# Kernel tuning notes

Hardware: AMD Instinct MI355X
Metric: run time of the kernel (lower is better)

## Reference

```python
import jax, jax.numpy as jnp
import numpy as np

# ---- constants from the source module ----
NB = [[0,1,2,3],[0,1,4],[0,2,5],[0,3,6],[1,4,7],[2,5,8],[3,6,9],[4,7,10],[5,8,11],[6,9],[7,10],[8,11],[12,13,14,15],[12,13,16],[12,14,17],[12,15],[13,16,18],[14,17,19],[16,18,20],[17,19,21],[18,20,22],[19,21,23],[20,22],[21,23]]
PARENT = np.array([0,0,0,0,1,2,3,4,5,6,7,8,9,9,9,12,13,14,16,17,18,19,20,21])  # root parent sentinel handled separately
KJ, NV, PREG = 24, 6890, 200
LEN = np.array([len(n) for n in NB])
NBR_IDX = np.zeros((KJ,4), np.int32)
NBR_VALID = np.zeros((KJ,4), np.float32)
for k, n in enumerate(NB):
    NBR_IDX[k,:len(n)] = n; NBR_VALID[k,:len(n)] = 1.0
BETA_POS = np.zeros((KJ,17), np.float32); BETA_POS[np.arange(KJ), 4*LEN] = 1.0
SLICE_MASK = np.zeros((23,17), np.float32)
for j in range(23):
    SLICE_MASK[j,:4*LEN[j]+1] = 1.0  # self.K[j] has 4*len(NB[j])+1 rows
NBR_IDX = jnp.asarray(NBR_IDX); NBR_VALID = jnp.asarray(NBR_VALID)
BETA_POS = jnp.asarray(BETA_POS); SLICE_MASK = jnpp = jnp.asarray(SLICE_MASK)


def setup_inputs() -> dict:
    key = jax.random.key(0)
    ks = jax.random.split(key, 9)
    V = jax.random.normal(ks[0], (PREG, NV, 3), jnp.float32)
    T = jax.random.normal(ks[1], (PREG, NV, 3), jnp.float32)
    J = jax.random.normal(ks[2], (PREG, KJ, 3), jnp.float32)
    theta = 0.3 * jax.random.normal(ks[3], (PREG, 72), jnp.float32)
    W_prime = jax.random.uniform(ks[4], (NV, KJ), jnp.float32)
    W_i = jax.random.uniform(ks[5], (NV, KJ), jnp.float32)
    W_i = W_i / W_i.sum(axis=1, keepdims=True)
    A = jax.random.uniform(ks[6], (23, NV), jnp.float32)
    K_mats = 0.01 * jax.random.normal(ks[7], (23, 17, 3 * NV), jnp.float32)
    K_mats = K_mats * SLICE_MASK[:, :, None]  # zero rows beyond the ragged per-joint size
    beta_2 = jnp.ones((1,), jnp.float32)
    return {"V": V, "T": T, "J": J, "theta": theta, "W_prime": W_prime, "W_i": W_i, "A": A, "K_mats": K_mats, "beta_2": beta_2, "epoch": 1}


def _rodrigues(pose):  # pose: (K,3)
    angle = jnp.maximum(jnp.linalg.norm(pose, axis=1, keepdims=True), 1e-8)
    axis = pose / angle
    x, y, z = axis[:, 0], axis[:, 1], axis[:, 2]
    zero = jnp.zeros_like(x)
    skew = jnp.stack([zero, -z, y, z, zero, -x, -y, x, zero], axis=1).reshape(-1, 3, 3)
    outer = axis[:, :, None] * axis[:, None, :]
    c = jnp.cos(angle)[:, :, None]
    s = jnp.sin(angle)[:, :, None]
    eye = jnp.eye(3, dtype=pose.dtype)[None]
    return c * eye + (1.0 - c) * outer + s * skew


def _compute_G(pose72, Jp):  # pose72: (72,), Jp: (K,3) -> (K,4,4)
    R = _rodrigues(pose72.reshape(KJ, 3))
    t = Jp - jnp.concatenate([jnp.zeros((1, 3), Jp.dtype), Jp[PARENT[1:]]], axis=0)
    G_local = jnp.zeros((KJ, 4, 4), Jp.dtype)
    G_local = G_local.at[:, :3, :3].set(R).at[:, :3, 3].set(t).at[:, 3, 3].set(1.0)
    Gs = [G_local[0]]
    for i in range(1, KJ):  # fixed 24-joint kinematic tree
        Gs.append(Gs[PARENT[i]] @ G_local[i])
    G = jnp.stack(Gs, axis=0)
    off = jnp.einsum('kij,kj->ki', G[:, :3, :3], Jp)  # homogeneous w=0 -> rotation only
    return G.at[:, :3, 3].add(-off)


def _axis2quat(p):  # (M,3) -> (M,4)
    angle = jnp.sqrt(jnp.maximum(jnp.sum(p ** 2, axis=1), 1e-16))
    n = p / angle[:, None]
    s = jnp.sin(angle / 2)
    return jnp.stack([n[:, 0] * s, n[:, 1] * s, n[:, 2] * s, jnp.cos(angle / 2) - 1.0], axis=1)


def reference(V, T, J, theta, W_prime, W_i, A, K_mats, beta_2, epoch):
    P = V.shape[0]
    b2 = beta_2[0]
    # normalized skinning weights
    W_relu = jax.nn.relu(W_prime)
    W_change = W_relu / (W_relu.sum(axis=1, keepdims=True) + 1e-8)
    # per-pose global joint transforms
    G_prime = jax.vmap(_compute_G)(theta, J)  # (P,K,4,4)
    # quaternion features and blend-shape correction
    q = _axis2quat(theta.reshape(P * KJ, 3)).reshape(P, KJ, 4)
    qg = q[:, NBR_IDX, :] * NBR_VALID[None, :, :, None]       # (P,K,4,4) neighbor gather
    q17 = jnp.concatenate([qg.reshape(P, KJ, 16), jnp.zeros((P, KJ, 1), q.dtype)], axis=-1)
    q17 = q17 + BETA_POS[None] * b2                            # beta_2 at column 4*len
    qm = q17[:, 1:, :] * SLICE_MASK[None]                      # ragged slice q_ne[:, j+1, :lenK]
    contrib = jnp.einsum('pjl,jlm->pjm', qm, K_mats).reshape(P, 23, NV, 3)
    T_p = jnp.einsum('pjnc,jn->pnc', contrib, jax.nn.relu(A)) + T
    # linear blend skinning
    T_h = jnp.concatenate([T_p, jnp.ones((P, NV, 1), T_p.dtype)], axis=-1)
    transformed = jnp.einsum('pkij,pnj->pnki', G_prime[:, :, :3, :], T_h)  # (P,N,K,3)
    verts = jnp.einsum('nk,pnkc->pnc', W_change, transformed)
    # energies
    e = float(epoch)
    g_wi = 0.1 * np.exp(-0.1 * e)
    g_w = 0.002 * np.exp(-0.008 * e)
    g_a = 0.001 * np.exp(-0.008 * e)
    g_k = 0.1 * np.exp(-0.008 * e)
    E_D = jnp.sum((V - verts) ** 2)
    E_Wi = jnp.sum((W_change - W_i) ** 2)
    E_W = jnp.sum(jnp.abs(W_change))
    E_A = jnp.sum(jnp.abs(A))
    E_K = jnp.sum(jnp.sqrt(jnp.sum(K_mats ** 2, axis=(1, 2))))
    E = E_D + g_wi * E_Wi + g_w * E_W + g_a * E_A + g_k * E_K
    return (E, verts)
```

## Files before the change

kernel.cpp:

```cpp
#include <hip/hip_runtime.h>
#include <math.h>

#define KJ 24
#define NV 6890
#define PREG 200
#define M_TOT (NV*3)
#define KDIM 391
#define KPAD 416
#define TP_STRIDE 20672
#define NMT64 323
#define NSTAGE (NMT64*13)

#define EDP_OFF 0
#define EKP_OFF 5400
#define WIP_OFF 101984
#define EWP_OFF 102016
#define EAP_OFF 102048
#define RED_OFF 102080
#define G_OFF   102112
#define TP_OFF  159712
#define QBH_OFF_U 10903488
#define QBL_OFF_U 11009984
#define BTH_OFF_U 11116480
#define BTL_OFF_U 19716032
#define TP2_OFF 14157792

typedef __attribute__((ext_vector_type(8))) short short8;
typedef __attribute__((ext_vector_type(4))) float f32x4;
typedef __attribute__((ext_vector_type(4))) unsigned int u32x4;

__constant__ int c_PARENT[24] = {0,0,0,0,1,2,3,4,5,6,7,8,9,9,9,12,13,14,16,17,18,19,20,21};
__constant__ int c_DEPTH[24]  = {0,1,1,1,2,2,2,3,3,3,4,4,4,4,4,5,5,5,6,6,7,7,8,8};
__constant__ int c_LEN[24]    = {4,3,3,3,3,3,3,3,3,2,2,2,4,3,3,2,3,3,3,3,3,3,2,2};
__constant__ int c_NBR[24][4] = {
  {0,1,2,3},{0,1,4,0},{0,2,5,0},{0,3,6,0},{1,4,7,0},{2,5,8,0},{3,6,9,0},{4,7,10,0},
  {5,8,11,0},{6,9,0,0},{7,10,0,0},{8,11,0,0},{12,13,14,15},{12,13,16,0},{12,14,17,0},
  {12,15,0,0},{13,16,18,0},{14,17,19,0},{16,18,20,0},{17,19,21,0},{18,20,22,0},
  {19,21,23,0},{20,22,0,0},{21,23,0,0}};

__device__ __forceinline__ float waveReduce(float v) {
  #pragma unroll
  for (int off = 32; off > 0; off >>= 1) v += __shfl_down(v, off, 64);
  return v;
}
__device__ __forceinline__ unsigned short f2bf(float x) {
  union { float f; unsigned u; } v; v.f = x;
  unsigned r = v.u + 0x7FFFu + ((v.u >> 16) & 1u);
  return (unsigned short)(r >> 16);
}
__device__ __forceinline__ float bf2f(unsigned short h) {
  union { unsigned u; float f; } v; v.u = ((unsigned)h) << 16; return v.f;
}

__global__ __launch_bounds__(256) void kPre(const float* __restrict__ J,
                                            const float* __restrict__ theta,
                                            const float* __restrict__ beta2,
                                            const float* __restrict__ Wp,
                                            const float* __restrict__ Wi,
                                            const float* __restrict__ A,
                                            const float* __restrict__ K,
                                            float* __restrict__ ws) {
  unsigned short* qbh = (unsigned short*)ws + QBH_OFF_U;
  unsigned short* qbl = (unsigned short*)ws + QBL_OFF_U;
  int b = blockIdx.x;
  if (b < 50) {
    __shared__ float Gl[4][24][12];
    __shared__ float Gg[4][24][12];
    __shared__ float q[4][24][4];
    int w = threadIdx.x >> 6, t = threadIdx.x & 63;
    int p = b*4 + w;
    if (t < 24) {
      float x = theta[p*72 + 3*t + 0];
      float y = theta[p*72 + 3*t + 1];
      float z = theta[p*72 + 3*t + 2];
      float n2 = x*x + y*y + z*z;
      float ang = fmaxf(sqrtf(n2), 1e-8f);
      float ia = 1.f/ang;
      float ax = x*ia, ay = y*ia, az = z*ia;
      float c = cosf(ang), s = sinf(ang), C = 1.f - c;
      float jx = J[p*72+3*t], jy = J[p*72+3*t+1], jz = J[p*72+3*t+2];
      float tx = jx, ty = jy, tz = jz;
      if (t > 0) {
        int par = c_PARENT[t];
        tx -= J[p*72+3*par]; ty -= J[p*72+3*par+1]; tz -= J[p*72+3*par+2];
      }
      Gl[w][t][0]=c+C*ax*ax;   Gl[w][t][1]=C*ax*ay-s*az; Gl[w][t][2]=C*ax*az+s*ay; Gl[w][t][3]=tx;
      Gl[w][t][4]=C*ax*ay+s*az;Gl[w][t][5]=c+C*ay*ay;    Gl[w][t][6]=C*ay*az-s*ax; Gl[w][t][7]=ty;
      Gl[w][t][8]=C*ax*az-s*ay;Gl[w][t][9]=C*ay*az+s*ax; Gl[w][t][10]=c+C*az*az;   Gl[w][t][11]=tz;
      float ang2 = sqrtf(fmaxf(n2, 1e-16f));
      float inv2 = 1.f/ang2;
      float s2 = sinf(0.5f*ang2);
      q[w][t][0] = x*inv2*s2; q[w][t][1] = y*inv2*s2; q[w][t][2] = z*inv2*s2;
      q[w][t][3] = cosf(0.5f*ang2) - 1.f;
    }
    __syncthreads();
    for (int lev = 0; lev <= 8; lev++) {
      if (t < 24 && c_DEPTH[t] == lev) {
        if (lev == 0) {
          for (int i2 = 0; i2 < 12; i2++) Gg[w][0][i2] = Gl[w][0][i2];
        } else {
          int par = c_PARENT[t];
          for (int r = 0; r < 3; r++) {
            float g0 = Gg[w][par][r*4+0], g1 = Gg[w][par][r*4+1];
            float g2 = Gg[w][par][r*4+2], g3 = Gg[w][par][r*4+3];
            for (int c2 = 0; c2 < 4; c2++) {
              float v = g0*Gl[w][t][0+c2] + g1*Gl[w][t][4+c2] + g2*Gl[w][t][8+c2];
              if (c2 == 3) v += g3;
              Gg[w][t][r*4+c2] = v;
            }
          }
        }
      }
      __syncthreads();
    }
    if (t < 24) {
      float jx = J[p*72+3*t], jy = J[p*72+3*t+1], jz = J[p*72+3*t+2];
      float* gp = ws + G_OFF + p*288 + t*12;
      #pragma unroll
      for (int r = 0; r < 3; r++) {
        float off = Gg[w][t][r*4+0]*jx + Gg[w][t][r*4+1]*jy + Gg[w][t][r*4+2]*jz;
        Gg[w][t][r*4+3] -= off;
      }
      #pragma unroll
      for (int i2 = 0; i2 < 12; i2++) gp[i2] = Gg[w][t][i2];
    }
    __syncthreads();
    float b2 = beta2[0];
    for (int e = t; e < KDIM; e += 64) {
      int j = e / 17, l = e - 17*j;
      int k = j + 1;
      float val = 0.f;
      if (l < 4*c_LEN[j] + 1) {
        if (l < 16) {
          int sidx = l >> 2, cc = l & 3;
          if (sidx < c_LEN[k]) val = q[w][c_NBR[k][sidx]][cc];
        }
        if (l == 4*c_LEN[k]) val += b2;
      }
      unsigned short hi = f2bf(val);
      unsigned short lo = f2bf(val - bf2f(hi));
      qbh[p*KPAD + e] = hi;
      qbl[p*KPAD + e] = lo;
    }
    for (int e = KDIM + t; e < KPAD; e += 64) {
      qbh[p*KPAD + e] = 0; qbl[p*KPAD + e] = 0;
    }
  } else if (b < 77) {
    int d = b - 50;
    int t = threadIdx.x;
    int n = d*256 + t;
    float ewi = 0.f, ew = 0.f, ea = 0.f;
    if (n < NV) {
      float wv[24]; float sum = 0.f;
      const float4* wp4 = (const float4*)(Wp + n*24);
      #pragma unroll
      for (int i = 0; i < 6; i++) {
        float4 v4 = wp4[i];
        wv[4*i+0] = fmaxf(v4.x, 0.f); wv[4*i+1] = fmaxf(v4.y, 0.f);
        wv[4*i+2] = fmaxf(v4.z, 0.f); wv[4*i+3] = fmaxf(v4.w, 0.f);
        sum += wv[4*i+0]+wv[4*i+1]+wv[4*i+2]+wv[4*i+3];
      }
      float inv = 1.f/(sum + 1e-8f);
      #pragma unroll
      for (int k = 0; k < 24; k++) {
        float wc = wv[k]*inv;
        ew += fabsf(wc);
        float dd = wc - Wi[n*24+k];
        ewi += dd*dd;
      }
    }
    for (int i = d*256 + t; i < 23*NV; i += 27*256) ea += fabsf(A[i]);
    for (int i = d*256 + t; i < 56*KPAD; i += 27*256) {
      qbh[200*KPAD + i] = 0; qbl[200*KPAD + i] = 0;
    }
    __shared__ float red[3][4];
    int lane = t & 63, wv2 = t >> 6;
    ewi = waveReduce(ewi); ew = waveReduce(ew); ea = waveReduce(ea);
    if (lane == 0) { red[0][wv2] = ewi; red[1][wv2] = ew; red[2][wv2] = ea; }
    __syncthreads();
    if (t == 0) {
      ws[WIP_OFF + d] = red[0][0]+red[0][1]+red[0][2]+red[0][3];
      ws[EWP_OFF + d] = red[1][0]+red[1][1]+red[1][2]+red[1][3];
      ws[EAP_OFF + d] = red[2][0]+red[2][1]+red[2][2]+red[2][3];
    }
  } else {
    int flat = b - 77;
    int bx = flat % NMT64, by = flat / NMT64;
    int m0 = bx*64, kg0 = by*32;
    __shared__ unsigned short Sh[32*66];
    __shared__ unsigned short Sl[32*66];
    __shared__ float ek[23];
    int t = threadIdx.x;
    if (t < 23) ek[t] = 0.f;
    __syncthreads();
    int krow = t >> 3, mseg = (t & 7) * 8;
    int kg = kg0 + krow;
    int mm = m0 + mseg;
    float kv[8], wv[8]; float sq = 0.f;
    #pragma unroll
    for (int i = 0; i < 8; i++) { kv[i] = 0.f; wv[i] = 0.f; }
    if (kg < KDIM) {
      const float* kr = K + (size_t)kg*M_TOT + mm;
      if (mm + 7 < M_TOT) {
        float4 a4 = *(const float4*)kr; float4 b4 = *(const float4*)(kr+4);
        kv[0]=a4.x; kv[1]=a4.y; kv[2]=a4.z; kv[3]=a4.w;
        kv[4]=b4.x; kv[5]=b4.y; kv[6]=b4.z; kv[7]=b4.w;
      } else {
        #pragma unroll
        for (int i = 0; i < 8; i++) if (mm+i < M_TOT) kv[i] = kr[i];
      }
      int j = kg / 17;
      int nb = mm / 3;
      float av[4];
      #pragma unroll
      for (int i = 0; i < 4; i++)
        av[i] = (nb + i < NV) ? fmaxf(A[j*NV + nb + i], 0.f) : 0.f;
      #pragma unroll
      for (int i = 0; i < 8; i++) {
        float a = (mm+i < M_TOT) ? av[(mm+i)/3 - nb] : 0.f;
        wv[i] = kv[i]*a;
        sq = fmaf(kv[i], kv[i], sq);
      }
    }
    #pragma unroll
    for (int c = 0; c < 4; c++) {
      unsigned short h0 = f2bf(wv[2*c]),  h1 = f2bf(wv[2*c+1]);
      unsigned short l0 = f2bf(wv[2*c]   - bf2f(h0));
      unsigned short l1 = f2bf(wv[2*c+1] - bf2f(h1));
      *(unsigned*)&Sh[krow*66 + mseg + 2*c] = (unsigned)h0 | ((unsigned)h1 << 16);
      *(unsigned*)&Sl[krow*66 + mseg + 2*c] = (unsigned)l0 | ((unsigned)l1 << 16);
    }
    sq += __shfl_xor(sq, 1, 64);
    sq += __shfl_xor(sq, 2, 64);
    sq += __shfl_xor(sq, 4, 64);
    if ((t & 7) == 0 && kg < KDIM) atomicAdd(&ek[kg/17], sq);
    __syncthreads();
    int mrow = t >> 2, kq = t & 3;
    unsigned dh[4], dl[4];
    #pragma unroll
    for (int c2 = 0; c2 < 4; c2++) {
      unsigned short s0 = Sh[(kq*8 + 2*c2    )*66 + mrow];
      unsigned short s1 = Sh[(kq*8 + 2*c2 + 1)*66 + mrow];
      dh[c2] = (unsigned)s0 | ((unsigned)s1 << 16);
      unsigned short u0 = Sl[(kq*8 + 2*c2    )*66 + mrow];
      unsigned short u1 = Sl[(kq*8 + 2*c2 + 1)*66 + mrow];
      dl[c2] = (unsigned)u0 | ((unsigned)u1 << 16);
    }
    unsigned short* BtH = (unsigned short*)ws + BTH_OFF_U;
    unsigned short* BtL = (unsigned short*)ws + BTL_OFF_U;
    size_t o = (size_t)(m0 + mrow)*KPAD + kg0 + kq*8;
    *(u32x4*)(BtH + o) = (u32x4){dh[0], dh[1], dh[2], dh[3]};
    *(u32x4*)(BtL + o) = (u32x4){dl[0], dl[1], dl[2], dl[3]};
    if (t < 23) ws[EKP_OFF + t*NSTAGE + flat] = ek[t];
  }
}

template<int KS0, int NKS>
__device__ __forceinline__ void kb_body(const unsigned short* __restrict__ qbh,
                                        const unsigned short* __restrict__ qbl,
                                        const unsigned short* __restrict__ BtH,
                                        const unsigned short* __restrict__ BtL,
                                        short (*__restrict__ SBh)[64*40],
                                        short (*__restrict__ SBl)[64*40],
                                        float* __restrict__ TPd, int m0) {
  const int tid = threadIdx.x;
  const int w = tid >> 6, lane = tid & 63;
  const int r = lane & 15, qd = lane >> 4;

  f32x4 acc[4][4];
  #pragma unroll
  for (int h = 0; h < 4; h++)
    #pragma unroll
    for (int f = 0; f < 4; f++) acc[h][f] = (f32x4){0.f,0.f,0.f,0.f};

  int aofs[4];
  #pragma unroll
  for (int h = 0; h < 4; h++) aofs[h] = (w*64 + h*16 + r)*KPAD + KS0*32 + qd*8;

  const int srow = tid >> 2, sseg = tid & 3;
  const size_t gB = (size_t)(m0 + srow)*KPAD + KS0*32 + sseg*8;
  const int swr = srow*40 + sseg*8;

  short8 ah[2][4], al[2][4];
  short8 bsh[2], bsl[2];

  bsh[0] = *(const short8*)(BtH + gB);
  bsl[0] = *(const short8*)(BtL + gB);
  #pragma unroll
  for (int h = 0; h < 4; h++) {
    ah[0][h] = *(const short8*)(qbh + aofs[h]);
    al[0][h] = *(const short8*)(qbl + aofs[h]);
  }
  *(short8*)&SBh[0][swr] = bsh[0];
  *(short8*)&SBl[0][swr] = bsl[0];
  bsh[1] = *(const short8*)(BtH + gB + 32);
  bsl[1] = *(const short8*)(BtL + gB + 32);
  #pragma unroll
  for (int h = 0; h < 4; h++) {
    ah[1][h] = *(const short8*)(qbh + aofs[h] + 32);
    al[1][h] = *(const short8*)(qbl + aofs[h] + 32);
  }
  __syncthreads();

  #pragma unroll
  for (int ks = 0; ks < NKS; ks++) {
    const int cur = ks & 1, nxt = cur ^ 1;
    short8 bfh[4], bfl[4];
    #pragma unroll
    for (int f = 0; f < 4; f++) {
      bfh[f] = *(const short8*)&SBh[cur][(f*16 + r)*40 + qd*8];
      bfl[f] = *(const short8*)&SBl[cur][(f*16 + r)*40 + qd*8];
    }
    #pragma unroll
    for (int f = 0; f < 4; f++)
      #pragma unroll
      for (int h = 0; h < 4; h++) {
        acc[h][f] = __builtin_amdgcn_mfma_f32_16x16x32_bf16(ah[cur][h], bfh[f], acc[h][f], 0, 0, 0);
        acc[h][f] = __builtin_amdgcn_mfma_f32_16x16x32_bf16(ah[cur][h], bfl[f], acc[h][f], 0, 0, 0);
        acc[h][f] = __builtin_amdgcn_mfma_f32_16x16x32_bf16(al[cur][h], bfh[f], acc[h][f], 0, 0, 0);
      }
    if (ks + 1 < NKS) {
      *(short8*)&SBh[nxt][swr] = bsh[nxt];
      *(short8*)&SBl[nxt][swr] = bsl[nxt];
    }
    if (ks + 2 < NKS) {
      const int o = (ks + 2) * 32;
      bsh[cur] = *(const short8*)(BtH + gB + o);
      bsl[cur] = *(const short8*)(BtL + gB + o);
      #pragma unroll
      for (int h = 0; h < 4; h++) {
        ah[cur][h] = *(const short8*)(qbh + aofs[h] + o);
        al[cur][h] = *(const short8*)(qbl + aofs[h] + o);
      }
    }
    __syncthreads();
  }
  #pragma unroll
  for (int h = 0; h < 4; h++)
    #pragma unroll
    for (int f = 0; f < 4; f++)
      #pragma unroll
      for (int g = 0; g < 4; g++) {
        int p = w*64 + h*16 + qd*4 + g;
        if (p < PREG)
          TPd[(size_t)p*TP_STRIDE + m0 + f*16 + r] = acc[h][f][g];
      }
}

__global__ __launch_bounds__(256) void kB(float* __restrict__ ws) {
  __shared__ short SBh[2][64*40];
  __shared__ short SBl[2][64*40];
  const unsigned short* qbh = (const unsigned short*)ws + QBH_OFF_U;
  const unsigned short* qbl = (const unsigned short*)ws + QBL_OFF_U;
  const unsigned short* BtH = (const unsigned short*)ws + BTH_OFF_U;
  const unsigned short* BtL = (const unsigned short*)ws + BTL_OFF_U;
  const int m0 = blockIdx.x * 64;
  if (blockIdx.y == 0)
    kb_body<0, 7>(qbh, qbl, BtH, BtL, SBh, SBl, ws + TP_OFF, m0);
  else
    kb_body<7, 6>(qbh, qbl, BtH, BtL, SBh, SBl, ws + TP2_OFF, m0);
}

__global__ __launch_bounds__(256) void kC(const float* __restrict__ V,
                                          const float* __restrict__ T,
                                          const float* __restrict__ Wp,
                                          const float* __restrict__ ws,
                                          float* __restrict__ out) {
  int p = blockIdx.y;
  int n = blockIdx.x*256 + threadIdx.x;
  const float* __restrict__ gp = ws + G_OFF + (size_t)p*288;
  __shared__ float tmp[4];
  float ed = 0.f;
  if (n < NV) {
    float wv[24]; float sum = 0.f;
    const float4* wp4 = (const float4*)(Wp + n*24);
    #pragma unroll
    for (int i = 0; i < 6; i++) {
      float4 v4 = wp4[i];
      wv[4*i+0] = fmaxf(v4.x, 0.f); wv[4*i+1] = fmaxf(v4.y, 0.f);
      wv[4*i+2] = fmaxf(v4.z, 0.f); wv[4*i+3] = fmaxf(v4.w, 0.f);
      sum += wv[4*i+0]+wv[4*i+1]+wv[4*i+2]+wv[4*i+3];
    }
    float inv = 1.f/(sum + 1e-8f);
    float M[12];
    #pragma unroll
    for (int i = 0; i < 12; i++) M[i] = 0.f;
    #pragma unroll
    for (int k = 0; k < 24; k++) {
      float wc = wv[k];
      #pragma unroll
      for (int i = 0; i < 12; i++)
        M[i] = fmaf(wc, gp[k*12 + i], M[i]);
    }
    #pragma unroll
    for (int i = 0; i < 12; i++) M[i] *= inv;
    size_t tb = (size_t)p*M_TOT + 3*n;
    size_t pb = (size_t)p*TP_STRIDE + 3*n;
    float t0 = ws[TP_OFF + pb + 0] + ws[TP2_OFF + pb + 0] + T[tb + 0];
    float t1 = ws[TP_OFF + pb + 1] + ws[TP2_OFF + pb + 1] + T[tb + 1];
    float t2 = ws[TP_OFF + pb + 2] + ws[TP2_OFF + pb + 2] + T[tb + 2];
    float v0 = M[0]*t0 + M[1]*t1 + M[2]*t2  + M[3];
    float v1 = M[4]*t0 + M[5]*t1 + M[6]*t2  + M[7];
    float v2 = M[8]*t0 + M[9]*t1 + M[10]*t2 + M[11];
    out[1+tb+0] = v0; out[1+tb+1] = v1; out[1+tb+2] = v2;
    float d0 = V[tb+0]-v0, d1 = V[tb+1]-v1, d2 = V[tb+2]-v2;
    ed = d0*d0 + d1*d1 + d2*d2;
  }
  ed = waveReduce(ed);
  int lane = threadIdx.x & 63, w = threadIdx.x >> 6;
  if (lane == 0) tmp[w] = ed;
  __syncthreads();
  if (threadIdx.x == 0)
    ((float*)ws)[EDP_OFF + blockIdx.y*27 + blockIdx.x] = tmp[0]+tmp[1]+tmp[2]+tmp[3];
}

__global__ __launch_bounds__(256) void kF1(float* __restrict__ ws) {
  __shared__ float sb[4];
  int b = blockIdx.x, t = threadIdx.x, lane = t & 63, w = t >> 6;
  if (b < 23) {
    float s = 0.f;
    for (int i = t; i < NSTAGE; i += 256) s += ws[EKP_OFF + b*NSTAGE + i];
    s = waveReduce(s);
    if (lane == 0) sb[w] = s;
    __syncthreads();
    if (t == 0) ws[RED_OFF + b] = sb[0]+sb[1]+sb[2]+sb[3];
  } else if (b == 23) {
    float s = 0.f;
    for (int i = t; i < 5400; i += 256) s += ws[EDP_OFF + i];
    s = waveReduce(s);
    if (lane == 0) sb[w] = s;
    __syncthreads();
    if (t == 0) ws[RED_OFF + 23] = sb[0]+sb[1]+sb[2]+sb[3];
  } else {
    if (w == 0) {
      float s = (lane < 27) ? ws[WIP_OFF + lane] : 0.f;
      s = waveReduce(s);
      if (lane == 0) ws[RED_OFF + 24] = s;
    } else if (w == 1) {
      float s = (lane < 27) ? ws[EWP_OFF + lane] : 0.f;
      s = waveReduce(s);
      if (lane == 0) ws[RED_OFF + 25] = s;
    } else if (w == 2) {
      float s = (lane < 27) ? ws[EAP_OFF + lane] : 0.f;
      s = waveReduce(s);
      if (lane == 0) ws[RED_OFF + 26] = s;
    }
  }
}

__global__ void kF2(const int* __restrict__ epoch, const float* __restrict__ ws,
                    float* __restrict__ out) {
  int t = threadIdx.x;
  float s = (t < 23) ? sqrtf(ws[RED_OFF + t]) : 0.f;
  s = waveReduce(s);
  if (t == 0) {
    float e    = (float)epoch[0];
    float g_wi = 0.1f   * expf(-0.1f  * e);
    float g_w  = 0.002f * expf(-0.008f* e);
    float g_a  = 0.001f * expf(-0.008f* e);
    float g_k  = 0.1f   * expf(-0.008f* e);
    out[0] = ws[RED_OFF+23] + g_wi*ws[RED_OFF+24] + g_w*ws[RED_OFF+25]
           + g_a*ws[RED_OFF+26] + g_k*s;
  }
}

extern "C" void kernel_launch(void* const* d_in, const int* in_sizes, int n_in,
                              void* d_out, int out_size, void* d_ws, size_t ws_size,
                              hipStream_t stream) {
  const float* V     = (const float*)d_in[0];
  const float* T     = (const float*)d_in[1];
  const float* J     = (const float*)d_in[2];
  const float* theta = (const float*)d_in[3];
  const float* Wp    = (const float*)d_in[4];
  const float* Wi    = (const float*)d_in[5];
  const float* A     = (const float*)d_in[6];
  const float* K     = (const float*)d_in[7];
  const float* b2    = (const float*)d_in[8];
  const int*   epoch = (const int*)d_in[9];
  float* out = (float*)d_out;
  float* ws  = (float*)d_ws;

  hipLaunchKernelGGL(kPre, dim3(77 + NSTAGE), dim3(256), 0, stream,
                     J, theta, b2, Wp, Wi, A, K, ws);
  hipLaunchKernelGGL(kB,   dim3(NMT64, 2),    dim3(256), 0, stream, ws);
  hipLaunchKernelGGL(kC,   dim3(27, PREG),    dim3(256), 0, stream, V, T, Wp, ws, out);
  hipLaunchKernelGGL(kF1,  dim3(25),          dim3(256), 0, stream, ws);
  hipLaunchKernelGGL(kF2,  dim3(1),           dim3(64),  0, stream, epoch, ws, out);
}
```

Baseline: 182.2 us.

## Widen GEMM tile to 128 columns, split K three ways, batch poses in skinning

The MFMA GEMM kernel now uses 512-thread blocks covering 128 output columns, with 8 waves each handling 32 pose rows. The K dimension is split into three partial sums instead of two, which adds a third partial buffer. The skinning kernel processes 8 poses per block and reuses the loaded blend weights across them, cutting the grid and the partial energy count. The goal is more B-tile reuse and fewer redundant weight loads. The cost is extra partial-buffer traffic, and the tile no longer divides M evenly, so loads and stores need clamping and guards.

```diff
diff --git a/kernel.cpp b/kernel.cpp
--- a/kernel.cpp
+++ b/kernel.cpp
@@ -10,6 +10,7 @@
 #define TP_STRIDE 20672
 #define NMT64 323
 #define NSTAGE (NMT64*13)
+#define NMT128 162
 
 #define EDP_OFF 0
 #define EKP_OFF 5400
@@ -24,6 +25,7 @@
 #define BTH_OFF_U 11116480
 #define BTL_OFF_U 19716032
 #define TP2_OFF 14157792
+#define TP3_OFF 19449824
 
 typedef __attribute__((ext_vector_type(8))) short short8;
 typedef __attribute__((ext_vector_type(4))) float f32x4;
@@ -260,34 +262,35 @@
                                         const unsigned short* __restrict__ qbl,
                                         const unsigned short* __restrict__ BtH,
                                         const unsigned short* __restrict__ BtL,
-                                        short (*__restrict__ SBh)[64*40],
-                                        short (*__restrict__ SBl)[64*40],
+                                        short (*__restrict__ SBh)[128*40],
+                                        short (*__restrict__ SBl)[128*40],
                                         float* __restrict__ TPd, int m0) {
   const int tid = threadIdx.x;
   const int w = tid >> 6, lane = tid & 63;
   const int r = lane & 15, qd = lane >> 4;
 
-  f32x4 acc[4][4];
-  #pragma unroll
-  for (int h = 0; h < 4; h++)
-    #pragma unroll
-    for (int f = 0; f < 4; f++) acc[h][f] = (f32x4){0.f,0.f,0.f,0.f};
-
-  int aofs[4];
-  #pragma unroll
-  for (int h = 0; h < 4; h++) aofs[h] = (w*64 + h*16 + r)*KPAD + KS0*32 + qd*8;
+  f32x4 acc[2][8];
+  #pragma unroll
+  for (int h = 0; h < 2; h++)
+    #pragma unroll
+    for (int f = 0; f < 8; f++) acc[h][f] = (f32x4){0.f,0.f,0.f,0.f};
+
+  int aofs[2];
+  #pragma unroll
+  for (int h = 0; h < 2; h++) aofs[h] = (w*32 + h*16 + r)*KPAD + KS0*32 + qd*8;
 
   const int srow = tid >> 2, sseg = tid & 3;
-  const size_t gB = (size_t)(m0 + srow)*KPAD + KS0*32 + sseg*8;
+  int grow = m0 + srow; if (grow > M_TOT + 1) grow = M_TOT + 1;
+  const size_t gB = (size_t)grow*KPAD + KS0*32 + sseg*8;
   const int swr = srow*40 + sseg*8;
 
-  short8 ah[2][4], al[2][4];
+  short8 ah[2][2], al[2][2];
   short8 bsh[2], bsl[2];
 
   bsh[0] = *(const short8*)(BtH + gB);
   bsl[0] = *(const short8*)(BtL + gB);
   #pragma unroll
-  for (int h = 0; h < 4; h++) {
+  for (int h = 0; h < 2; h++) {
     ah[0][h] = *(const short8*)(qbh + aofs[h]);
     al[0][h] = *(const short8*)(qbl + aofs[h]);
   }
@@ -296,7 +299,7 @@
   bsh[1] = *(const short8*)(BtH + gB + 32);
   bsl[1] = *(const short8*)(BtL + gB + 32);
   #pragma unroll
-  for (int h = 0; h < 4; h++) {
+  for (int h = 0; h < 2; h++) {
     ah[1][h] = *(const short8*)(qbh + aofs[h] + 32);
     al[1][h] = *(const short8*)(qbl + aofs[h] + 32);
   }
@@ -305,16 +308,16 @@
   #pragma unroll
   for (int ks = 0; ks < NKS; ks++) {
     const int cur = ks & 1, nxt = cur ^ 1;
-    short8 bfh[4], bfl[4];
-    #pragma unroll
-    for (int f = 0; f < 4; f++) {
+    short8 bfh[8], bfl[8];
+    #pragma unroll
+    for (int f = 0; f < 8; f++) {
       bfh[f] = *(const short8*)&SBh[cur][(f*16 + r)*40 + qd*8];
       bfl[f] = *(const short8*)&SBl[cur][(f*16 + r)*40 + qd*8];
     }
     #pragma unroll
-    for (int f = 0; f < 4; f++)
-      #pragma unroll
-      for (int h = 0; h < 4; h++) {
+    for (int f = 0; f < 8; f++)
+      #pragma unroll
+      for (int h = 0; h < 2; h++) {
         acc[h][f] = __builtin_amdgcn_mfma_f32_16x16x32_bf16(ah[cur][h], bfh[f], acc[h][f], 0, 0, 0);
         acc[h][f] = __builtin_amdgcn_mfma_f32_16x16x32_bf16(ah[cur][h], bfl[f], acc[h][f], 0, 0, 0);
         acc[h][f] = __builtin_amdgcn_mfma_f32_16x16x32_bf16(al[cur][h], bfh[f], acc[h][f], 0, 0, 0);
@@ -328,7 +331,7 @@
       bsh[cur] = *(const short8*)(BtH + gB + o);
       bsl[cur] = *(const short8*)(BtL + gB + o);
       #pragma unroll
-      for (int h = 0; h < 4; h++) {
+      for (int h = 0; h < 2; h++) {
         ah[cur][h] = *(const short8*)(qbh + aofs[h] + o);
         al[cur][h] = *(const short8*)(qbl + aofs[h] + o);
       }
@@ -336,29 +339,35 @@
     __syncthreads();
   }
   #pragma unroll
-  for (int h = 0; h < 4; h++)
-    #pragma unroll
-    for (int f = 0; f < 4; f++)
-      #pragma unroll
-      for (int g = 0; g < 4; g++) {
-        int p = w*64 + h*16 + qd*4 + g;
-        if (p < PREG)
-          TPd[(size_t)p*TP_STRIDE + m0 + f*16 + r] = acc[h][f][g];
-      }
-}
-
-__global__ __launch_bounds__(256) void kB(float* __restrict__ ws) {
-  __shared__ short SBh[2][64*40];
-  __shared__ short SBl[2][64*40];
+  for (int h = 0; h < 2; h++)
+    #pragma unroll
+    for (int f = 0; f < 8; f++) {
+      int mc = m0 + f*16 + r;
+      if (mc < TP_STRIDE) {
+        #pragma unroll
+        for (int g = 0; g < 4; g++) {
+          int p = w*32 + h*16 + qd*4 + g;
+          if (p < PREG)
+            TPd[(size_t)p*TP_STRIDE + mc] = acc[h][f][g];
+        }
+      }
+    }
+}
+
+__global__ __launch_bounds__(512) void kB(float* __restrict__ ws) {
+  __shared__ short SBh[2][128*40];
+  __shared__ short SBl[2][128*40];
   const unsigned short* qbh = (const unsigned short*)ws + QBH_OFF_U;
   const unsigned short* qbl = (const unsigned short*)ws + QBL_OFF_U;
   const unsigned short* BtH = (const unsigned short*)ws + BTH_OFF_U;
   const unsigned short* BtL = (const unsigned short*)ws + BTL_OFF_U;
-  const int m0 = blockIdx.x * 64;
+  const int m0 = blockIdx.x * 128;
   if (blockIdx.y == 0)
-    kb_body<0, 7>(qbh, qbl, BtH, BtL, SBh, SBl, ws + TP_OFF, m0);
+    kb_body<0, 5>(qbh, qbl, BtH, BtL, SBh, SBl, ws + TP_OFF, m0);
+  else if (blockIdx.y == 1)
+    kb_body<5, 4>(qbh, qbl, BtH, BtL, SBh, SBl, ws + TP2_OFF, m0);
   else
-    kb_body<7, 6>(qbh, qbl, BtH, BtL, SBh, SBl, ws + TP2_OFF, m0);
+    kb_body<9, 4>(qbh, qbl, BtH, BtL, SBh, SBl, ws + TP3_OFF, m0);
 }
 
 __global__ __launch_bounds__(256) void kC(const float* __restrict__ V,
@@ -366,9 +375,8 @@
                                           const float* __restrict__ Wp,
                                           const float* __restrict__ ws,
                                           float* __restrict__ out) {
-  int p = blockIdx.y;
+  int p0 = blockIdx.y * 8;
   int n = blockIdx.x*256 + threadIdx.x;
-  const float* __restrict__ gp = ws + G_OFF + (size_t)p*288;
   __shared__ float tmp[4];
   float ed = 0.f;
   if (n < NV) {
@@ -382,29 +390,33 @@
       sum += wv[4*i+0]+wv[4*i+1]+wv[4*i+2]+wv[4*i+3];
     }
     float inv = 1.f/(sum + 1e-8f);
-    float M[12];
-    #pragma unroll
-    for (int i = 0; i < 12; i++) M[i] = 0.f;
-    #pragma unroll
-    for (int k = 0; k < 24; k++) {
-      float wc = wv[k];
-      #pragma unroll
-      for (int i = 0; i < 12; i++)
-        M[i] = fmaf(wc, gp[k*12 + i], M[i]);
-    }
-    #pragma unroll
-    for (int i = 0; i < 12; i++) M[i] *= inv;
-    size_t tb = (size_t)p*M_TOT + 3*n;
-    size_t pb = (size_t)p*TP_STRIDE + 3*n;
-    float t0 = ws[TP_OFF + pb + 0] + ws[TP2_OFF + pb + 0] + T[tb + 0];
-    float t1 = ws[TP_OFF + pb + 1] + ws[TP2_OFF + pb + 1] + T[tb + 1];
-    float t2 = ws[TP_OFF + pb + 2] + ws[TP2_OFF + pb + 2] + T[tb + 2];
-    float v0 = M[0]*t0 + M[1]*t1 + M[2]*t2  + M[3];
-    float v1 = M[4]*t0 + M[5]*t1 + M[6]*t2  + M[7];
-    float v2 = M[8]*t0 + M[9]*t1 + M[10]*t2 + M[11];
-    out[1+tb+0] = v0; out[1+tb+1] = v1; out[1+tb+2] = v2;
-    float d0 = V[tb+0]-v0, d1 = V[tb+1]-v1, d2 = V[tb+2]-v2;
-    ed = d0*d0 + d1*d1 + d2*d2;
+    for (int pp = 0; pp < 8; pp++) {
+      int p = p0 + pp;
+      const float* __restrict__ gp = ws + G_OFF + (size_t)p*288;
+      float M[12];
+      #pragma unroll
+      for (int i = 0; i < 12; i++) M[i] = 0.f;
+      #pragma unroll
+      for (int k = 0; k < 24; k++) {
+        float wc = wv[k];
+        #pragma unroll
+        for (int i = 0; i < 12; i++)
+          M[i] = fmaf(wc, gp[k*12 + i], M[i]);
+      }
+      #pragma unroll
+      for (int i = 0; i < 12; i++) M[i] *= inv;
+      size_t tb = (size_t)p*M_TOT + 3*n;
+      size_t pb = (size_t)p*TP_STRIDE + 3*n;
+      float t0 = ws[TP_OFF + pb + 0] + ws[TP2_OFF + pb + 0] + ws[TP3_OFF + pb + 0] + T[tb + 0];
+      float t1 = ws[TP_OFF + pb + 1] + ws[TP2_OFF + pb + 1] + ws[TP3_OFF + pb + 1] + T[tb + 1];
+      float t2 = ws[TP_OFF + pb + 2] + ws[TP2_OFF + pb + 2] + ws[TP3_OFF + pb + 2] + T[tb + 2];
+      float v0 = M[0]*t0 + M[1]*t1 + M[2]*t2  + M[3];
+      float v1 = M[4]*t0 + M[5]*t1 + M[6]*t2  + M[7];
+      float v2 = M[8]*t0 + M[9]*t1 + M[10]*t2 + M[11];
+      out[1+tb+0] = v0; out[1+tb+1] = v1; out[1+tb+2] = v2;
+      float d0 = V[tb+0]-v0, d1 = V[tb+1]-v1, d2 = V[tb+2]-v2;
+      ed += d0*d0 + d1*d1 + d2*d2;
+    }
   }
   ed = waveReduce(ed);
   int lane = threadIdx.x & 63, w = threadIdx.x >> 6;
@@ -426,7 +438,7 @@
     if (t == 0) ws[RED_OFF + b] = sb[0]+sb[1]+sb[2]+sb[3];
   } else if (b == 23) {
     float s = 0.f;
-    for (int i = t; i < 5400; i += 256) s += ws[EDP_OFF + i];
+    for (int i = t; i < 675; i += 256) s += ws[EDP_OFF + i];
     s = waveReduce(s);
     if (lane == 0) sb[w] = s;
     __syncthreads();
@@ -482,8 +494,8 @@
 
   hipLaunchKernelGGL(kPre, dim3(77 + NSTAGE), dim3(256), 0, stream,
                      J, theta, b2, Wp, Wi, A, K, ws);
-  hipLaunchKernelGGL(kB,   dim3(NMT64, 2),    dim3(256), 0, stream, ws);
-  hipLaunchKernelGGL(kC,   dim3(27, PREG),    dim3(256), 0, stream, V, T, Wp, ws, out);
+  hipLaunchKernelGGL(kB,   dim3(NMT128, 3),   dim3(512), 0, stream, ws);
+  hipLaunchKernelGGL(kC,   dim3(27, 25),      dim3(256), 0, stream, V, T, Wp, ws, out);
   hipLaunchKernelGGL(kF1,  dim3(25),          dim3(256), 0, stream, ws);
   hipLaunchKernelGGL(kF2,  dim3(1),           dim3(64),  0, stream, epoch, ws, out);
 }
```

New measurement: 185.4 us. No clear change (+1.7%).
